# Kernel optimization log

Measured on AMD Instinct MI355X. Metric: run time of the kernel, lower is better.

Reference implementation:

```python
import jax, jax.numpy as jnp
import numpy as np

B, N, K = 4, 4096, 16
DIN, DOUT = 64, 64


def _gather(points, idx):
    # points: [B, N, F], idx: [B, M, K] -> [B, M, K, F]
    return jax.vmap(lambda p, i: p[i])(points, idx)


def setup_inputs() -> dict:
    key = jax.random.key(0)
    ks = jax.random.split(key, 20)
    s = 0.05
    inp = {
        "coordinates": jax.random.normal(ks[0], (B, N, 3), dtype=jnp.float32),
        "features": jax.random.normal(ks[1], (B, N, DIN), dtype=jnp.float32),
        "w1": jax.random.normal(ks[2], (DIN, DOUT), jnp.float32) * s,
        "b1": jnp.zeros((DOUT,), jnp.float32),
        "w2": jax.random.normal(ks[3], (DOUT, DIN), jnp.float32) * s,
        "b2": jnp.zeros((DIN,), jnp.float32),
        "wq": jax.random.normal(ks[4], (DOUT, DOUT), jnp.float32) * s,
        "wk": jax.random.normal(ks[5], (DOUT, DOUT), jnp.float32) * s,
        "wv": jax.random.normal(ks[6], (DOUT, DOUT), jnp.float32) * s,
        "wm1": jax.random.normal(ks[7], (DOUT, DOUT), jnp.float32) * s,
        "bm1": jnp.zeros((DOUT,), jnp.float32),
        "wm2": jax.random.normal(ks[8], (DOUT, DOUT), jnp.float32) * s,
        "bm2": jnp.zeros((DOUT,), jnp.float32),
        "wp1": jax.random.normal(ks[9], (3, DOUT), jnp.float32) * s,
        "bp1": jnp.zeros((DOUT,), jnp.float32),
        "wp2": jax.random.normal(ks[10], (DOUT, DOUT), jnp.float32) * s,
        "bp2": jnp.zeros((DOUT,), jnp.float32),
    }
    return inp


def reference(coordinates, features, w1, b1, w2, b2, wq, wk, wv,
              wm1, bm1, wm2, bm2, wp1, bp1, wp2, bp2):
    # Full pairwise squared distances [B, N, N]
    diff = coordinates[:, :, None, :] - coordinates[:, None, :, :]
    dists = jnp.sum(diff * diff, axis=-1)
    # k smallest distances == argsort()[..., :k]
    _, knn_idx = jax.lax.top_k(-dists, K)            # [B, N, K]

    knn_coords = _gather(coordinates, knn_idx)       # [B, N, K, 3]

    x = features @ w1 + b1                           # [B, N, DOUT]
    q = x @ wq
    k_g = _gather(x @ wk, knn_idx)                   # [B, N, K, DOUT]
    v_g = _gather(x @ wv, knn_idx)

    rel = coordinates[:, :, None, :] - knn_coords    # [B, N, K, 3]
    pos_enc = jax.nn.relu(rel @ wp1 + bp1) @ wp2 + bp2

    attn = q[:, :, None, :] - k_g + pos_enc
    attn = jax.nn.relu(attn @ wm1 + bm1) @ wm2 + bm2
    attn = jax.nn.softmax(attn / np.sqrt(DOUT).astype(np.float32), axis=-2)

    out = jnp.einsum("bmnf,bmnf->bmf", attn, v_g + pos_enc)
    out = out @ w2 + b2 + features
    return (out, attn)
```

## Files before the change

kernel.cpp:

```cpp
#include <hip/hip_runtime.h>
#include <hip/hip_bf16.h>

#define BATCH 4
#define NPTS 4096
#define KNBR 16
#define D 64
#define NQ (BATCH * NPTS)
#define QPW 2
#define PT_QPW 4

using short8 = __attribute__((ext_vector_type(8))) short;
using short4v = __attribute__((ext_vector_type(4))) short;
using f32x4 = __attribute__((ext_vector_type(4))) float;

__device__ __forceinline__ float rl(float v, int i) {
  return __int_as_float(__builtin_amdgcn_readlane(__float_as_int(v), i));
}
__device__ __forceinline__ short f2bf(float x) {
  __hip_bfloat16 h = __float2bfloat16(x);
  return *reinterpret_cast<short*>(&h);
}
__device__ __forceinline__ float bf2f(short s) {
  union { unsigned u; float f; } v;
  v.u = ((unsigned)(unsigned short)s) << 16;
  return v.f;
}
#define MFMA16(a, b, c) __builtin_amdgcn_mfma_f32_16x16x32_bf16(a, b, c, 0, 0, 0)

#define INF_KEY 0x7F800000FFFFFFFFull

__device__ __forceinline__ unsigned long long bitonic64(unsigned long long v, int lane) {
#pragma unroll
  for (int k = 2; k <= 64; k <<= 1) {
#pragma unroll
    for (int j = k >> 1; j > 0; j >>= 1) {
      unsigned long long o = __shfl_xor(v, j);
      const bool up = (lane & k) == 0;
      const bool lower = (lane & j) == 0;
      unsigned long long mn = v < o ? v : o;
      unsigned long long mx = v < o ? o : v;
      v = (up == lower) ? mn : mx;
    }
  }
  return v;
}

__global__ __launch_bounds__(256, 8) void knn_kernel(const float* __restrict__ coords,
                                                     int* __restrict__ knn) {
  __shared__ unsigned long long buf[4][QPW][64];
  __shared__ int cnt[4][QPW];
  const int t = threadIdx.x;
  const int w = t >> 6, lane = t & 63;
  const int qbase = blockIdx.x * (4 * QPW) + w * QPW;
  const int b = qbase >> 12;
  const float* cb = coords + (size_t)b * NPTS * 3;

  float qx[QPW], qy[QPW], qz[QPW];
  unsigned long long m[QPW];
#pragma unroll
  for (int q = 0; q < QPW; ++q) {
    const int qi = (qbase + q) & (NPTS - 1);
    qx[q] = cb[(size_t)qi * 3];
    qy[q] = cb[(size_t)qi * 3 + 1];
    qz[q] = cb[(size_t)qi * 3 + 2];
    m[q] = INF_KEY;
  }

#pragma unroll 4
  for (int s = 0; s < 64; ++s) {
    const int j = s * 64 + lane;
    const float px = cb[3 * j], py = cb[3 * j + 1], pz = cb[3 * j + 2];
#pragma unroll
    for (int q = 0; q < QPW; ++q) {
      float dx = __fsub_rn(qx[q], px);
      float dy = __fsub_rn(qy[q], py);
      float dz = __fsub_rn(qz[q], pz);
      float d = __fadd_rn(__fadd_rn(__fmul_rn(dx, dx), __fmul_rn(dy, dy)), __fmul_rn(dz, dz));
      unsigned long long key = ((unsigned long long)__float_as_uint(d) << 32) | (unsigned)j;
      m[q] = key < m[q] ? key : m[q];
    }
  }
  unsigned long long K16[QPW];
#pragma unroll
  for (int q = 0; q < QPW; ++q) K16[q] = __shfl(bitonic64(m[q], lane), 15);
  if (lane < QPW) cnt[w][lane] = 0;

#pragma unroll 4
  for (int s = 0; s < 64; ++s) {
    const int j = s * 64 + lane;
    const float px = cb[3 * j], py = cb[3 * j + 1], pz = cb[3 * j + 2];
#pragma unroll
    for (int q = 0; q < QPW; ++q) {
      float dx = __fsub_rn(qx[q], px);
      float dy = __fsub_rn(qy[q], py);
      float dz = __fsub_rn(qz[q], pz);
      float d = __fadd_rn(__fadd_rn(__fmul_rn(dx, dx), __fmul_rn(dy, dy)), __fmul_rn(dz, dz));
      unsigned long long key = ((unsigned long long)__float_as_uint(d) << 32) | (unsigned)j;
      if (key <= K16[q]) {
        int slot = atomicAdd(&cnt[w][q], 1);
        if (slot < 64) buf[w][q][slot] = key;
      }
    }
  }
#pragma unroll
  for (int q = 0; q < QPW; ++q) {
    const int n = cnt[w][q];
    unsigned long long v = (lane < n) ? buf[w][q][lane] : INF_KEY;
    v = bitonic64(v, lane);
    if (lane < 16) knn[(size_t)(qbase + q) * 16 + lane] = (int)(v & 0xFFFFFFFFu);
  }
}

#define FT_RPT 8
__global__ __launch_bounds__(256) void ft_kernel(const float* __restrict__ feat,
    const float* __restrict__ w1, const float* __restrict__ b1,
    const float* __restrict__ wq, const float* __restrict__ wk, const float* __restrict__ wv,
    float* __restrict__ qo, float* __restrict__ ko, float* __restrict__ vo) {
  __shared__ float W[4][D * D];
  const int t = threadIdx.x;
  {
    const float4* s0 = (const float4*)w1;
    const float4* s1 = (const float4*)wq;
    const float4* s2 = (const float4*)wk;
    const float4* s3 = (const float4*)wv;
    for (int c = t; c < D * D / 4; c += 256) {
      ((float4*)W[0])[c] = s0[c]; ((float4*)W[1])[c] = s1[c];
      ((float4*)W[2])[c] = s2[c]; ((float4*)W[3])[c] = s3[c];
    }
  }
  __syncthreads();
  const int f = t & 63, w = t >> 6;
  const float b1f = b1[f];
  const int gw = blockIdx.x * 4 + w;
  for (int r = 0; r < FT_RPT; ++r) {
    const int row = gw * FT_RPT + r;
    const float fv = feat[(size_t)row * D + f];
    float x = b1f;
#pragma unroll
    for (int i = 0; i < D; ++i) x = fmaf(rl(fv, i), W[0][i * D + f], x);
    float q = 0.f, kk = 0.f, vv = 0.f;
#pragma unroll
    for (int i = 0; i < D; ++i) {
      float xi = rl(x, i);
      q  = fmaf(xi, W[1][i * D + f], q);
      kk = fmaf(xi, W[2][i * D + f], kk);
      vv = fmaf(xi, W[3][i * D + f], vv);
    }
    qo[(size_t)row * D + f] = q;
    ko[(size_t)row * D + f] = kk;
    vo[(size_t)row * D + f] = vv;
  }
}

__global__ __launch_bounds__(256, 4) void pt_kernel(const float* __restrict__ coords,
    const float* __restrict__ feat,
    const float* __restrict__ qws, const float* __restrict__ kws, const float* __restrict__ vws,
    const int* __restrict__ knn,
    const float* __restrict__ wp1, const float* __restrict__ bp1,
    const float* __restrict__ wp2, const float* __restrict__ bp2,
    const float* __restrict__ wm1, const float* __restrict__ bm1,
    const float* __restrict__ wm2, const float* __restrict__ bm2,
    const float* __restrict__ w2g, const float* __restrict__ b2,
    float* __restrict__ out, float* __restrict__ attn_g) {
  __shared__ short WBp[512 * 8], WBm1[512 * 8], WBm2[512 * 8];
  __shared__ float wp1t[D * 4];
  __shared__ float biases[4 * D];
  __shared__ int knnq[4][PT_QPW][16];
  __shared__ short xch[4][16][72];

  const int t = threadIdx.x;
  for (int s = t; s < 512 * 3; s += 256) {
    const int m = s >> 9, rem = s & 511;
    const int tk = rem >> 6, l = rem & 63;
    const int tt = tk >> 1, ks = tk & 1;
    const float* src = (m == 0) ? wp2 : ((m == 1) ? wm1 : wm2);
    short* dst = (m == 0) ? WBp : ((m == 1) ? WBm1 : WBm2);
#pragma unroll
    for (int j = 0; j < 8; ++j) {
      const int k = ((l >> 4) << 3) + j + (ks << 5);
      const int n = (l & 15) + (tt << 4);
      dst[rem * 8 + j] = f2bf(src[k * D + n]);
    }
  }
  if (t < 64) {
    wp1t[t * 4 + 0] = wp1[t];
    wp1t[t * 4 + 1] = wp1[D + t];
    wp1t[t * 4 + 2] = wp1[2 * D + t];
    wp1t[t * 4 + 3] = bp1[t];
    biases[t] = bp2[t]; biases[64 + t] = bm1[t];
    biases[128 + t] = bm2[t]; biases[192 + t] = b2[t];
  }
  const int w = t >> 6, lane = t & 63;
  const int qbase0 = blockIdx.x * (4 * PT_QPW) + w * PT_QPW;
  {
    const int q = lane >> 4, k = lane & 15;
    const int qi = qbase0 + q;
    const int bbase = (qi >> 12) << 12;
    knnq[w][q][k] = bbase + knn[(size_t)qi * 16 + k];
  }
  __syncthreads();

  const int l15 = lane & 15, g = lane >> 4;
  float ovq[PT_QPW];

  for (int q = 0; q < PT_QPW; ++q) {
    const int qi = qbase0 + q;
    const int gjA = knnq[w][q][l15];
    const float qx = coords[(size_t)qi * 3], qy = coords[(size_t)qi * 3 + 1], qz = coords[(size_t)qi * 3 + 2];
    const float rx = qx - coords[(size_t)gjA * 3];
    const float ry = qy - coords[(size_t)gjA * 3 + 1];
    const float rz = qz - coords[(size_t)gjA * 3 + 2];
    short8 ha[2];
#pragma unroll
    for (int ks = 0; ks < 2; ++ks) {
#pragma unroll
      for (int j = 0; j < 8; ++j) {
        const int c = g * 8 + j + ks * 32;
        const float4 wv = *(const float4*)&wp1t[c * 4];
        float h = fmaf(rx, wv.x, fmaf(ry, wv.y, fmaf(rz, wv.z, wv.w)));
        ha[ks][j] = f2bf(fmaxf(h, 0.f));
      }
    }
    f32x4 pe_d[4];
#pragma unroll
    for (int tt = 0; tt < 4; ++tt) {
      f32x4 acc = {0.f, 0.f, 0.f, 0.f};
      acc = MFMA16(ha[0], *(const short8*)&WBp[((tt * 2 + 0) * 64 + lane) * 8], acc);
      acc = MFMA16(ha[1], *(const short8*)&WBp[((tt * 2 + 1) * 64 + lane) * 8], acc);
      const float bb = biases[l15 + tt * 16];
#pragma unroll
      for (int r = 0; r < 4; ++r) {
        pe_d[tt][r] = acc[r] + bb;
        xch[w][4 * g + r][l15 + 16 * tt] = f2bf(pe_d[tt][r]);
      }
    }
    __syncthreads();
    short8 aa[2];
#pragma unroll
    for (int ks = 0; ks < 2; ++ks) {
      const int c0 = g * 8 + ks * 32;
      const float4 q0 = *(const float4*)&qws[(size_t)qi * D + c0];
      const float4 q1 = *(const float4*)&qws[(size_t)qi * D + c0 + 4];
      const float4 k0 = *(const float4*)&kws[(size_t)gjA * D + c0];
      const float4 k1 = *(const float4*)&kws[(size_t)gjA * D + c0 + 4];
      const short8 pv = *(const short8*)&xch[w][l15][c0];
      aa[ks][0] = f2bf(q0.x - k0.x + bf2f(pv[0]));
      aa[ks][1] = f2bf(q0.y - k0.y + bf2f(pv[1]));
      aa[ks][2] = f2bf(q0.z - k0.z + bf2f(pv[2]));
      aa[ks][3] = f2bf(q0.w - k0.w + bf2f(pv[3]));
      aa[ks][4] = f2bf(q1.x - k1.x + bf2f(pv[4]));
      aa[ks][5] = f2bf(q1.y - k1.y + bf2f(pv[5]));
      aa[ks][6] = f2bf(q1.z - k1.z + bf2f(pv[6]));
      aa[ks][7] = f2bf(q1.w - k1.w + bf2f(pv[7]));
    }
#pragma unroll
    for (int tt = 0; tt < 4; ++tt) {
      f32x4 acc = {0.f, 0.f, 0.f, 0.f};
      acc = MFMA16(aa[0], *(const short8*)&WBm1[((tt * 2 + 0) * 64 + lane) * 8], acc);
      acc = MFMA16(aa[1], *(const short8*)&WBm1[((tt * 2 + 1) * 64 + lane) * 8], acc);
      const float bb = biases[64 + l15 + tt * 16];
#pragma unroll
      for (int r = 0; r < 4; ++r)
        xch[w][4 * g + r][l15 + 16 * tt] = f2bf(fmaxf(acc[r] + bb, 0.f));
    }
    __syncthreads();
    const short8 a20 = *(const short8*)&xch[w][l15][g * 8];
    const short8 a21 = *(const short8*)&xch[w][l15][g * 8 + 32];
    f32x4 s3[4];
#pragma unroll
    for (int tt = 0; tt < 4; ++tt) {
      f32x4 acc = {0.f, 0.f, 0.f, 0.f};
      acc = MFMA16(a20, *(const short8*)&WBm2[((tt * 2 + 0) * 64 + lane) * 8], acc);
      acc = MFMA16(a21, *(const short8*)&WBm2[((tt * 2 + 1) * 64 + lane) * 8], acc);
      const float bb = biases[128 + l15 + tt * 16];
#pragma unroll
      for (int r = 0; r < 4; ++r) s3[tt][r] = acc[r] + bb;
    }
    float att[4][4];
#pragma unroll
    for (int tt = 0; tt < 4; ++tt) {
      float v0 = s3[tt][0] * 0.125f, v1 = s3[tt][1] * 0.125f;
      float v2 = s3[tt][2] * 0.125f, v3 = s3[tt][3] * 0.125f;
      float mx = fmaxf(fmaxf(v0, v1), fmaxf(v2, v3));
      mx = fmaxf(mx, __shfl_xor(mx, 16));
      mx = fmaxf(mx, __shfl_xor(mx, 32));
      float e0 = __expf(v0 - mx), e1 = __expf(v1 - mx), e2 = __expf(v2 - mx), e3 = __expf(v3 - mx);
      float sm = (e0 + e1) + (e2 + e3);
      sm += __shfl_xor(sm, 16);
      sm += __shfl_xor(sm, 32);
      const float inv = 1.0f / sm;
      att[tt][0] = e0 * inv; att[tt][1] = e1 * inv;
      att[tt][2] = e2 * inv; att[tt][3] = e3 * inv;
    }
    __syncthreads();
#pragma unroll
    for (int tt = 0; tt < 4; ++tt)
#pragma unroll
      for (int r = 0; r < 4; ++r)
        xch[w][4 * g + r][l15 + 16 * tt] = f2bf(att[tt][r]);
    __syncthreads();
    {
      float* aq = attn_g + (size_t)qi * KNBR * D;
#pragma unroll
      for (int k = 0; k < 4; ++k) {
        const short4v sv = *(const short4v*)&xch[w][g + 4 * k][4 * l15];
        float4 fv;
        fv.x = bf2f(sv.x); fv.y = bf2f(sv.y); fv.z = bf2f(sv.z); fv.w = bf2f(sv.w);
        *(float4*)(aq + lane * 4 + k * 256) = fv;
      }
    }
    float ovp[4] = {0.f, 0.f, 0.f, 0.f};
#pragma unroll
    for (int r = 0; r < 4; ++r) {
      const int gjr = knnq[w][q][4 * g + r];
#pragma unroll
      for (int tt = 0; tt < 4; ++tt) {
        const float vv = vws[(size_t)gjr * D + l15 + 16 * tt];
        ovp[tt] = fmaf(att[tt][r], vv + pe_d[tt][r], ovp[tt]);
      }
    }
#pragma unroll
    for (int tt = 0; tt < 4; ++tt) {
      ovp[tt] += __shfl_xor(ovp[tt], 16);
      ovp[tt] += __shfl_xor(ovp[tt], 32);
    }
    ovq[q] = (g == 0) ? ovp[0] : ((g == 1) ? ovp[1] : ((g == 2) ? ovp[2] : ovp[3]));
  }

  float o2[PT_QPW];
#pragma unroll
  for (int q = 0; q < PT_QPW; ++q) o2[q] = biases[192 + lane];
#pragma unroll 8
  for (int i = 0; i < D; ++i) {
    const float wv = w2g[i * D + lane];
#pragma unroll
    for (int q = 0; q < PT_QPW; ++q) o2[q] = fmaf(rl(ovq[q], i), wv, o2[q]);
  }
#pragma unroll
  for (int q = 0; q < PT_QPW; ++q) {
    const int qi = qbase0 + q;
    out[(size_t)qi * D + lane] = o2[q] + feat[(size_t)qi * D + lane];
  }
}

extern "C" void kernel_launch(void* const* d_in, const int* in_sizes, int n_in,
                              void* d_out, int out_size, void* d_ws, size_t ws_size,
                              hipStream_t stream) {
  const float* coords = (const float*)d_in[0];
  const float* feat   = (const float*)d_in[1];
  const float* w1  = (const float*)d_in[2];
  const float* b1  = (const float*)d_in[3];
  const float* w2  = (const float*)d_in[4];
  const float* b2  = (const float*)d_in[5];
  const float* wq  = (const float*)d_in[6];
  const float* wk  = (const float*)d_in[7];
  const float* wv  = (const float*)d_in[8];
  const float* wm1 = (const float*)d_in[9];
  const float* bm1 = (const float*)d_in[10];
  const float* wm2 = (const float*)d_in[11];
  const float* bm2 = (const float*)d_in[12];
  const float* wp1 = (const float*)d_in[13];
  const float* bp1 = (const float*)d_in[14];
  const float* wp2 = (const float*)d_in[15];
  const float* bp2 = (const float*)d_in[16];

  int* knn = (int*)d_ws;
  float* qws = (float*)((char*)d_ws + (size_t)1 * (1 << 20));
  float* kws = (float*)((char*)d_ws + (size_t)5 * (1 << 20));
  float* vws = (float*)((char*)d_ws + (size_t)9 * (1 << 20));
  float* out  = (float*)d_out;
  float* attn = out + (size_t)NQ * D;

  hipLaunchKernelGGL(knn_kernel, dim3(NQ / (4 * QPW)), dim3(256), 0, stream,
                     coords, knn);
  hipLaunchKernelGGL(ft_kernel, dim3(NQ / (4 * FT_RPT)), dim3(256), 0, stream,
                     feat, w1, b1, wq, wk, wv, qws, kws, vws);
  hipLaunchKernelGGL(pt_kernel, dim3(NQ / (4 * PT_QPW)), dim3(256), 0, stream,
                     coords, feat, qws, kws, vws, knn,
                     wp1, bp1, wp2, bp2, wm1, bm1, wm2, bm2, w2, b2, out, attn);
}
```

Measured before the change: 125.1 us.

## Compute feature transform projections with bf16 MFMA instead of scalar FMAs

Rewrites the feature-transform kernel so the x = feat·w1 + b1 projection and the q/k/v projections run on bf16 MFMA 16x16 tiles. Weights are converted to bf16 and stored in shared memory in MFMA operand layout, and the intermediate x is exchanged through a shared buffer. This is meant to cut the scalar FMA and readlane cost of the small GEMMs. In exchange, inputs and weights are rounded to bf16, which may reduce accuracy, and every block now repacks all four weight matrices on entry.

```diff
diff --git a/kernel.cpp b/kernel.cpp
--- a/kernel.cpp
+++ b/kernel.cpp
@@ -111,44 +111,85 @@
   }
 }
 
-#define FT_RPT 8
 __global__ __launch_bounds__(256) void ft_kernel(const float* __restrict__ feat,
     const float* __restrict__ w1, const float* __restrict__ b1,
     const float* __restrict__ wq, const float* __restrict__ wk, const float* __restrict__ wv,
     float* __restrict__ qo, float* __restrict__ ko, float* __restrict__ vo) {
-  __shared__ float W[4][D * D];
+  __shared__ short W1b[512 * 8], Wqb[512 * 8], Wkb[512 * 8], Wvb[512 * 8];
+  __shared__ float b1s[D];
+  __shared__ short xch[4][16][72];
   const int t = threadIdx.x;
-  {
-    const float4* s0 = (const float4*)w1;
-    const float4* s1 = (const float4*)wq;
-    const float4* s2 = (const float4*)wk;
-    const float4* s3 = (const float4*)wv;
-    for (int c = t; c < D * D / 4; c += 256) {
-      ((float4*)W[0])[c] = s0[c]; ((float4*)W[1])[c] = s1[c];
-      ((float4*)W[2])[c] = s2[c]; ((float4*)W[3])[c] = s3[c];
-    }
-  }
+  for (int s = t; s < 512 * 4; s += 256) {
+    const int m = s >> 9, rem = s & 511;
+    const int tk = rem >> 6, l = rem & 63;
+    const int tt = tk >> 1, ks = tk & 1;
+    const float* src = (m == 0) ? w1 : ((m == 1) ? wq : ((m == 2) ? wk : wv));
+    short* dst = (m == 0) ? W1b : ((m == 1) ? Wqb : ((m == 2) ? Wkb : Wvb));
+#pragma unroll
+    for (int j = 0; j < 8; ++j) {
+      const int k = ((l >> 4) << 3) + j + (ks << 5);
+      const int n = (l & 15) + (tt << 4);
+      dst[rem * 8 + j] = f2bf(src[k * D + n]);
+    }
+  }
+  if (t < 64) b1s[t] = b1[t];
   __syncthreads();
-  const int f = t & 63, w = t >> 6;
-  const float b1f = b1[f];
-  const int gw = blockIdx.x * 4 + w;
-  for (int r = 0; r < FT_RPT; ++r) {
-    const int row = gw * FT_RPT + r;
-    const float fv = feat[(size_t)row * D + f];
-    float x = b1f;
-#pragma unroll
-    for (int i = 0; i < D; ++i) x = fmaf(rl(fv, i), W[0][i * D + f], x);
-    float q = 0.f, kk = 0.f, vv = 0.f;
-#pragma unroll
-    for (int i = 0; i < D; ++i) {
-      float xi = rl(x, i);
-      q  = fmaf(xi, W[1][i * D + f], q);
-      kk = fmaf(xi, W[2][i * D + f], kk);
-      vv = fmaf(xi, W[3][i * D + f], vv);
-    }
-    qo[(size_t)row * D + f] = q;
-    ko[(size_t)row * D + f] = kk;
-    vo[(size_t)row * D + f] = vv;
+
+  const int w = t >> 6, lane = t & 63;
+  const int l15 = lane & 15, g = lane >> 4;
+  const int row0 = blockIdx.x * 64 + w * 16;
+
+  short8 fa[2];
+#pragma unroll
+  for (int ks = 0; ks < 2; ++ks) {
+    const int c0 = g * 8 + ks * 32;
+    const float4 f0 = *(const float4*)&feat[(size_t)(row0 + l15) * D + c0];
+    const float4 f1 = *(const float4*)&feat[(size_t)(row0 + l15) * D + c0 + 4];
+    fa[ks][0] = f2bf(f0.x); fa[ks][1] = f2bf(f0.y);
+    fa[ks][2] = f2bf(f0.z); fa[ks][3] = f2bf(f0.w);
+    fa[ks][4] = f2bf(f1.x); fa[ks][5] = f2bf(f1.y);
+    fa[ks][6] = f2bf(f1.z); fa[ks][7] = f2bf(f1.w);
+  }
+#pragma unroll
+  for (int tt = 0; tt < 4; ++tt) {
+    f32x4 acc = {0.f, 0.f, 0.f, 0.f};
+    acc = MFMA16(fa[0], *(const short8*)&W1b[((tt * 2 + 0) * 64 + lane) * 8], acc);
+    acc = MFMA16(fa[1], *(const short8*)&W1b[((tt * 2 + 1) * 64 + lane) * 8], acc);
+    const float bb = b1s[l15 + tt * 16];
+#pragma unroll
+    for (int r = 0; r < 4; ++r)
+      xch[w][4 * g + r][l15 + 16 * tt] = f2bf(acc[r] + bb);
+  }
+  __syncthreads();
+  const short8 xa0 = *(const short8*)&xch[w][l15][g * 8];
+  const short8 xa1 = *(const short8*)&xch[w][l15][g * 8 + 32];
+
+#pragma unroll
+  for (int tt = 0; tt < 4; ++tt) {
+    f32x4 acc = {0.f, 0.f, 0.f, 0.f};
+    acc = MFMA16(xa0, *(const short8*)&Wqb[((tt * 2 + 0) * 64 + lane) * 8], acc);
+    acc = MFMA16(xa1, *(const short8*)&Wqb[((tt * 2 + 1) * 64 + lane) * 8], acc);
+#pragma unroll
+    for (int r = 0; r < 4; ++r)
+      qo[(size_t)(row0 + 4 * g + r) * D + l15 + 16 * tt] = acc[r];
+  }
+#pragma unroll
+  for (int tt = 0; tt < 4; ++tt) {
+    f32x4 acc = {0.f, 0.f, 0.f, 0.f};
+    acc = MFMA16(xa0, *(const short8*)&Wkb[((tt * 2 + 0) * 64 + lane) * 8], acc);
+    acc = MFMA16(xa1, *(const short8*)&Wkb[((tt * 2 + 1) * 64 + lane) * 8], acc);
+#pragma unroll
+    for (int r = 0; r < 4; ++r)
+      ko[(size_t)(row0 + 4 * g + r) * D + l15 + 16 * tt] = acc[r];
+  }
+#pragma unroll
+  for (int tt = 0; tt < 4; ++tt) {
+    f32x4 acc = {0.f, 0.f, 0.f, 0.f};
+    acc = MFMA16(xa0, *(const short8*)&Wvb[((tt * 2 + 0) * 64 + lane) * 8], acc);
+    acc = MFMA16(xa1, *(const short8*)&Wvb[((tt * 2 + 1) * 64 + lane) * 8], acc);
+#pragma unroll
+    for (int r = 0; r < 4; ++r)
+      vo[(size_t)(row0 + 4 * g + r) * D + l15 + 16 * tt] = acc[r];
   }
 }
 
@@ -373,7 +414,7 @@
 
   hipLaunchKernelGGL(knn_kernel, dim3(NQ / (4 * QPW)), dim3(256), 0, stream,
                      coords, knn);
-  hipLaunchKernelGGL(ft_kernel, dim3(NQ / (4 * FT_RPT)), dim3(256), 0, stream,
+  hipLaunchKernelGGL(ft_kernel, dim3(NQ / 64), dim3(256), 0, stream,
                      feat, w1, b1, wq, wk, wv, qws, kws, vws);
   hipLaunchKernelGGL(pt_kernel, dim3(NQ / (4 * PT_QPW)), dim3(256), 0, stream,
                      coords, feat, qws, kws, vws, knn,
```

After: 110.7 us. -11.5%, faster.
